# Kernel optimization log

Measured on AMD Instinct MI355X. Metric: run time of the kernel, lower is better.

Reference implementation:

```python
import jax, jax.numpy as jnp
import numpy as np

B, L = 8, 2048          # images, lines per image
C_IN, HW = 256, 128     # backbone feature channels, spatial size
DIM_LOI = 128
N_PTS0, N_PTS1 = 32, 8  # sampled points per line, after maxpool
SCALE = N_PTS0 // N_PTS1
EPS = 1e-5


def setup_inputs() -> dict:
    key = jax.random.key(0)
    ks = jax.random.split(key, 24)
    d = {}
    d['feature'] = jax.random.normal(ks[0], (B, C_IN, HW, HW), jnp.float32)
    # line endpoints in pixel coords [0, 128)
    d['lines'] = jax.random.uniform(ks[1], (B, L, 2, 2), jnp.float32) * HW
    # fc1: 1x1 conv 256 -> 128
    d['fc1_w'] = jax.random.normal(ks[2], (DIM_LOI, C_IN), jnp.float32) * 0.05
    d['fc1_b'] = jnp.zeros((DIM_LOI,), jnp.float32)
    planes = DIM_LOI // 2
    def bn(k, c):
        k1, k2, k3 = jax.random.split(k, 3)
        return (jax.random.normal(k1, (c,), jnp.float32) * 0.1 + 1.0,
                jax.random.normal(k2, (c,), jnp.float32) * 0.1,
                jax.random.normal(k3, (c,), jnp.float32) * 0.05,
                jax.random.uniform(jax.random.fold_in(k, 7), (c,), jnp.float32, 0.5, 1.5))
    d['bn1_g'], d['bn1_b'], d['bn1_m'], d['bn1_v'] = bn(ks[3], DIM_LOI)
    d['conv1_w'] = jax.random.normal(ks[4], (planes, DIM_LOI), jnp.float32) * 0.05
    d['conv1_b'] = jnp.zeros((planes,), jnp.float32)
    d['bn2_g'], d['bn2_b'], d['bn2_m'], d['bn2_v'] = bn(ks[5], planes)
    d['conv2_w'] = jax.random.normal(ks[6], (planes, planes, 3), jnp.float32) * 0.05
    d['conv2_b'] = jnp.zeros((planes,), jnp.float32)
    d['bn3_g'], d['bn3_b'], d['bn3_m'], d['bn3_v'] = bn(ks[7], planes)
    d['conv3_w'] = jax.random.normal(ks[8], (DIM_LOI, planes), jnp.float32) * 0.05
    d['conv3_b'] = jnp.zeros((DIM_LOI,), jnp.float32)
    d['fc2_w'] = jax.random.normal(ks[9], (1, DIM_LOI * N_PTS1), jnp.float32) * 0.02
    d['fc2_b'] = jnp.zeros((1,), jnp.float32)
    return d


def _bn(x, g, b, m, v):
    # x: [N, C, T], eval-mode batchnorm
    s = g * jax.lax.rsqrt(v + EPS)
    return x * s[None, :, None] + (b - m * s)[None, :, None]


def _loi_forward(feature, lines, fc1_w, fc1_b,
                 bn1_g, bn1_b, bn1_m, bn1_v, conv1_w, conv1_b,
                 bn2_g, bn2_b, bn2_m, bn2_v, conv2_w, conv2_b,
                 bn3_g, bn3_b, bn3_m, bn3_v, conv3_w, conv3_b,
                 fc2_w, fc2_b):
    # fc1: 1x1 conv -> [B, DIM_LOI, H, W]
    x = jnp.einsum('oc,bchw->bohw', fc1_w, feature) + fc1_b[None, :, None, None]

    # sample N_PTS0 points per line: p = p0*lam + p1*(1-lam) - 0.5
    lam = jnp.linspace(0.0, 1.0, N_PTS0, dtype=lines.dtype)  # [P]
    pts = (lines[:, :, 0, None, :] * lam[None, None, :, None]
           + lines[:, :, 1, None, :] * (1.0 - lam[None, None, :, None]) - 0.5)  # [B,L,P,2]
    px, py = pts[..., 0], pts[..., 1]
    px0 = jnp.clip(jnp.floor(px), 0.0, HW - 1.0)
    py0 = jnp.clip(jnp.floor(py), 0.0, HW - 1.0)
    px1 = jnp.clip(px0 + 1.0, 0.0, HW - 1.0)
    py1 = jnp.clip(py0 + 1.0, 0.0, HW - 1.0)
    px0l, py0l = px0.astype(jnp.int32), py0.astype(jnp.int32)
    px1l, py1l = px1.astype(jnp.int32), py1.astype(jnp.int32)

    def gather(f, ix, iy):  # f: [C,H,W], ix/iy: [L,P] -> [C,L,P]
        return f[:, ix, iy]

    gat = jax.vmap(gather)  # over batch
    xp = (gat(x, px0l, py0l) * ((px1 - px) * (py1 - py))[:, None]
          + gat(x, px1l, py0l) * ((px - px0) * (py1 - py))[:, None]
          + gat(x, px0l, py1l) * ((px1 - px) * (py - py0))[:, None]
          + gat(x, px1l, py1l) * ((px - px0) * (py - py0))[:, None])  # [B,C,L,P]

    xp = xp.transpose(0, 2, 1, 3).reshape(B * L, DIM_LOI, N_PTS0)  # [N,C,P]
    # MaxPool1d(kernel=stride=SCALE)
    xp = xp.reshape(B * L, DIM_LOI, N_PTS1, SCALE).max(axis=-1)  # [N,C,T=8]

    # Bottleneck1D residual: x + op(x)
    h = jax.nn.relu(_bn(xp, bn1_g, bn1_b, bn1_m, bn1_v))
    h = jnp.einsum('oc,nct->not', conv1_w, h) + conv1_b[None, :, None]
    h = jax.nn.relu(_bn(h, bn2_g, bn2_b, bn2_m, bn2_v))
    h = jax.lax.conv_general_dilated(h, conv2_w, (1,), [(1, 1)],
                                     dimension_numbers=('NCH', 'OIH', 'NCH'))
    h = h + conv2_b[None, :, None]
    h = jax.nn.relu(_bn(h, bn3_g, bn3_b, bn3_m, bn3_v))
    h = jnp.einsum('oc,nct->not', conv3_w, h) + conv3_b[None, :, None]
    xp = xp + h

    # fc2: ReLU -> Linear(dim_loi*n_pts1, 1)
    flat = jax.nn.relu(xp).reshape(B * L, DIM_LOI * N_PTS1)
    logits = (flat @ fc2_w.T + fc2_b).reshape(-1)  # [B*L]
    return logits


def reference(feature, lines, fc1_w, fc1_b,
              bn1_g, bn1_b, bn1_m, bn1_v, conv1_w, conv1_b,
              bn2_g, bn2_b, bn2_m, bn2_v, conv2_w, conv2_b,
              bn3_g, bn3_b, bn3_m, bn3_v, conv3_w, conv3_b,
              fc2_w, fc2_b):
    return _loi_forward(feature, lines, fc1_w, fc1_b,
                        bn1_g, bn1_b, bn1_m, bn1_v, conv1_w, conv1_b,
                        bn2_g, bn2_b, bn2_m, bn2_v, conv2_w, conv2_b,
                        bn3_g, bn3_b, bn3_m, bn3_v, conv3_w, conv3_b,
                        fc2_w, fc2_b)
```

## Files before the change

kernel.cpp:

```cpp
#include <hip/hip_runtime.h>

#define EPSBN 1e-5f

typedef _Float16 f16;
typedef _Float16 f16x8 __attribute__((ext_vector_type(8)));
typedef _Float16 f16x4 __attribute__((ext_vector_type(4)));
typedef _Float16 f16x2 __attribute__((ext_vector_type(2)));
typedef float    f32x4 __attribute__((ext_vector_type(4)));

__device__ inline unsigned int pack2(float a, float b) {
    union { f16x2 h; unsigned int u; } cv;
    cv.h[0] = (f16)a; cv.h[1] = (f16)b;
    return cv.u;
}
__device__ inline f16x4 hmax4(f16x4 a, f16x4 b) {
    f16x4 r;
    #pragma unroll
    for (int i = 0; i < 4; ++i) r[i] = a[i] > b[i] ? a[i] : b[i];
    return r;
}
__device__ inline f16x8 relu8(f16x8 v) {
    f16x8 r;
    #pragma unroll
    for (int i = 0; i < 8; ++i) r[i] = v[i] > (f16)0.f ? v[i] : (f16)0.f;
    return r;
}

__global__ void wprep_kernel(const float* __restrict__ fc1w,
                             const float* __restrict__ w1,
                             const float* __restrict__ w2,
                             const float* __restrict__ w3,
                             f16* __restrict__ dst) {
    const int i = blockIdx.x * 256 + threadIdx.x;
    float v;
    if (i < 32768)      v = fc1w[i];
    else if (i < 40960) v = w1[i - 32768];
    else if (i < 53248) {
        const int j = i - 40960, tau = j >> 12, rest = j & 4095;
        v = w2[rest * 3 + tau];
    } else              v = w3[i - 53248];
    dst[i] = (f16)v;
}

__global__ __launch_bounds__(512, 4)
void fc1_mfma(const float* __restrict__ feat,
              const f16*   __restrict__ w16,
              const float* __restrict__ bias,
              f16*         __restrict__ xmap) {
    __shared__ union {
        float fbuf[2][8368];
        f16   epi[256][136];
    } u;

    const int tid  = threadIdx.x;
    const int wv   = tid >> 6, lane = tid & 63;
    const int n16  = lane & 15, quad = lane >> 4;
    const int img  = blockIdx.x & 7;
    const int p0   = (blockIdx.x >> 3) << 8;

    const float* fimg = feat + (((size_t)img) << 22);

    f32x4 acc[8][2];
    #pragma unroll
    for (int ot = 0; ot < 8; ++ot) {
        acc[ot][0] = (f32x4){0.f, 0.f, 0.f, 0.f};
        acc[ot][1] = (f32x4){0.f, 0.f, 0.f, 0.f};
    }

    auto issue = [&](int s, int b) {
        #pragma unroll
        for (int i = 0; i < 4; ++i) {
            const int cl = wv * 4 + i;
            const int ch = s * 32 + cl;
            const float* src = fimg + (((size_t)ch) << 14) + p0 + lane * 4;
            float* dst = &u.fbuf[b][cl * 260 + (cl >> 3) * 16];
            __builtin_amdgcn_global_load_lds(
                (const __attribute__((address_space(1))) void*)src,
                (__attribute__((address_space(3))) void*)dst, 16, 0, 0);
        }
    };

    issue(0, 0);
    __syncthreads();

    for (int s = 0; s < 8; ++s) {
        const int cur = s & 1;
        if (s < 7) issue(s + 1, cur ^ 1);

        f16x8 xf[2];
        #pragma unroll
        for (int pt = 0; pt < 2; ++pt) {
            const int pbase = wv * 32 + pt * 16 + n16;
            const float* fb = &u.fbuf[cur][quad * 16 + pbase];
            f16x8 xv;
            #pragma unroll
            for (int j = 0; j < 8; ++j)
                xv[j] = (f16)fb[(quad * 8 + j) * 260];
            xf[pt] = xv;
        }

        const f16* wrow = w16 + (size_t)n16 * 256 + s * 32 + quad * 8;
        #pragma unroll
        for (int ot = 0; ot < 8; ++ot) {
            const f16x8 wf = *(const f16x8*)(wrow + ot * 4096);
            acc[ot][0] = __builtin_amdgcn_mfma_f32_16x16x32_f16(wf, xf[0], acc[ot][0], 0, 0, 0);
            acc[ot][1] = __builtin_amdgcn_mfma_f32_16x16x32_f16(wf, xf[1], acc[ot][1], 0, 0, 0);
        }
        __syncthreads();
    }

    #pragma unroll
    for (int ot = 0; ot < 8; ++ot) {
        const float4 bq = *(const float4*)&bias[ot * 16 + quad * 4];
        const float bqa[4] = {bq.x, bq.y, bq.z, bq.w};
        #pragma unroll
        for (int pt = 0; pt < 2; ++pt) {
            f16x4 h;
            #pragma unroll
            for (int r = 0; r < 4; ++r) h[r] = (f16)(acc[ot][pt][r] + bqa[r]);
            *(f16x4*)&u.epi[wv * 32 + pt * 16 + n16][ot * 16 + quad * 4] = h;
        }
    }
    __syncthreads();

    #pragma unroll
    for (int it = 0; it < 8; ++it) {
        const int idx = it * 512 + tid;
        const int row = idx >> 4, seg = idx & 15;
        const float4 v = *(const float4*)&u.epi[row][seg * 8];
        *(float4*)&xmap[(((size_t)(img * 16384 + p0 + row)) << 7) + seg * 8] = v;
    }
}

__global__ __launch_bounds__(256)
void loi_kernel(const f16*   __restrict__ x,
                const float* __restrict__ lines,
                const f16*   __restrict__ wsp,
                const float* __restrict__ bn1g, const float* __restrict__ bn1b,
                const float* __restrict__ bn1m, const float* __restrict__ bn1v,
                const float* __restrict__ b1,
                const float* __restrict__ bn2g, const float* __restrict__ bn2b,
                const float* __restrict__ bn2m, const float* __restrict__ bn2v,
                const float* __restrict__ b2,
                const float* __restrict__ bn3g, const float* __restrict__ bn3b,
                const float* __restrict__ bn3m, const float* __restrict__ bn3v,
                const float* __restrict__ b3,
                const float* __restrict__ fc2w, const float* __restrict__ fc2b,
                float* __restrict__ out) {
    __shared__ f16 xp[64][136];
    __shared__ alignas(16) union {
        struct { int toff[256][4]; f16 twgt[256][4]; } tp;
        struct { f16 h1[80][72]; f16 h2[64][72]; } cv;
    } u;
    __shared__ f16 s1h[128], t1h[128];
    __shared__ float s2f[64], t2f[64], s3f[64], t3f[64], b1f[64], b2f[64];
    __shared__ float b3f[128];
    __shared__ float wsum[4][8];

    const f16* w1f16 = wsp + 32768;
    const f16* w2f16 = wsp + 40960;
    const f16* w3f16 = wsp + 53248;

    const int tid  = threadIdx.x;
    const int wv   = tid >> 6, lane = tid & 63;
    const int n16  = lane & 15, quad = lane >> 4;
    const int img  = blockIdx.x & 7;
    const int mblk = blockIdx.x >> 3;

    if (tid < 128) {
        const float s = bn1g[tid] * rsqrtf(bn1v[tid] + EPSBN);
        s1h[tid] = (f16)s; t1h[tid] = (f16)(bn1b[tid] - bn1m[tid] * s);
    }
    if (tid < 64) {
        const float s = bn2g[tid] * rsqrtf(bn2v[tid] + EPSBN);
        s2f[tid] = s; t2f[tid] = bn2b[tid] - bn2m[tid] * s;
        b1f[tid] = b1[tid];
    } else if (tid < 128) {
        const int c = tid - 64;
        const float s = bn3g[c] * rsqrtf(bn3v[c] + EPSBN);
        s3f[c] = s; t3f[c] = bn3b[c] - bn3m[c] * s;
        b2f[c] = b2[c];
    } else {
        b3f[tid - 128] = b3[tid - 128];
    }

    {
        const int li = tid >> 5, pt = tid & 31;
        const int gl = img * 2048 + mblk * 8 + li;
        const float4 ln = *(const float4*)&lines[gl * 4];
        const float lam = (float)pt * (1.0f / 31.0f);
        const float px = ln.x * lam + ln.z * (1.f - lam) - 0.5f;
        const float py = ln.y * lam + ln.w * (1.f - lam) - 0.5f;
        const float px0 = fminf(fmaxf(floorf(px), 0.f), 127.f);
        const float py0 = fminf(fmaxf(floorf(py), 0.f), 127.f);
        const float px1 = fminf(px0 + 1.f, 127.f);
        const float py1 = fminf(py0 + 1.f, 127.f);
        const int ix0 = (int)px0, iy0 = (int)py0;
        const int ix1 = (int)px1, iy1 = (int)py1;
        u.tp.toff[tid][0] = (((ix0 << 7) + iy0) << 7);
        u.tp.toff[tid][1] = (((ix1 << 7) + iy0) << 7);
        u.tp.toff[tid][2] = (((ix0 << 7) + iy1) << 7);
        u.tp.toff[tid][3] = (((ix1 << 7) + iy1) << 7);
        const float wx1 = px1 - px, wx0 = px - px0;
        const float wy1 = py1 - py, wy0 = py - py0;
        u.tp.twgt[tid][0] = (f16)(wx1 * wy1); u.tp.twgt[tid][1] = (f16)(wx0 * wy1);
        u.tp.twgt[tid][2] = (f16)(wx1 * wy0); u.tp.twgt[tid][3] = (f16)(wx0 * wy0);
    }
    __syncthreads();

    {
        const int h = lane >> 5, j = lane & 31;
        const int li = wv * 2 + h;
        const f16* xbh = x + (((size_t)img) << 21) + 4 * j;
        #pragma unroll
        for (int t = 0; t < 8; ++t) {
            f16x4 m = {(f16)(-60000.f), (f16)(-60000.f), (f16)(-60000.f), (f16)(-60000.f)};
            #pragma unroll
            for (int s = 0; s < 4; ++s) {
                const int combo = li * 32 + t * 4 + s;
                const int4  off = *(const int4*)&u.tp.toff[combo][0];
                const f16x4 tw  = *(const f16x4*)&u.tp.twgt[combo][0];
                const f16x4 g00 = *(const f16x4*)(xbh + off.x);
                const f16x4 g10 = *(const f16x4*)(xbh + off.y);
                const f16x4 g01 = *(const f16x4*)(xbh + off.z);
                const f16x4 g11 = *(const f16x4*)(xbh + off.w);
                const f16x4 w0 = {tw[0], tw[0], tw[0], tw[0]};
                const f16x4 w1v = {tw[1], tw[1], tw[1], tw[1]};
                const f16x4 w2v = {tw[2], tw[2], tw[2], tw[2]};
                const f16x4 w3v = {tw[3], tw[3], tw[3], tw[3]};
                f16x4 v = g00 * w0 + g10 * w1v + g01 * w2v + g11 * w3v;
                m = hmax4(m, v);
            }
            *(f16x4*)&xp[li * 8 + t][4 * j] = m;
        }
    }
    __syncthreads();

    {
        const int r = tid >> 4, seg = tid & 15;
        const int row = (r >> 1) * 10 + (r & 1) * 9;
        *(unsigned long long*)&u.cv.h1[row][seg * 4] = 0ull;
    }

    {
        const int o_lane = wv * 16 + n16;
        f32x4 acc1[4];
        #pragma unroll
        for (int nt = 0; nt < 4; ++nt) acc1[nt] = (f32x4){0.f, 0.f, 0.f, 0.f};
        #pragma unroll
        for (int ks = 0; ks < 4; ++ks) {
            const int k = ks * 32 + quad * 8;
            const f16x8 a  = *(const f16x8*)&w1f16[o_lane * 128 + k];
            const f16x8 s8 = *(const f16x8*)&s1h[k];
            const f16x8 t8 = *(const f16x8*)&t1h[k];
            #pragma unroll
            for (int nt = 0; nt < 4; ++nt) {
                const f16x8 raw = *(const f16x8*)&xp[nt * 16 + n16][k];
                const f16x8 bf = relu8(raw * s8 + t8);
                acc1[nt] = __builtin_amdgcn_mfma_f32_16x16x32_f16(a, bf, acc1[nt], 0, 0, 0);
            }
        }
        #pragma unroll
        for (int nt = 0; nt < 4; ++nt) {
            const int n = nt * 16 + n16;
            const int nprow = (n >> 3) * 10 + (n & 7) + 1;
            #pragma unroll
            for (int r = 0; r < 4; ++r) {
                const int o = wv * 16 + quad * 4 + r;
                const float v = fmaxf((acc1[nt][r] + b1f[o]) * s2f[o] + t2f[o], 0.f);
                u.cv.h1[nprow][o] = (f16)v;
            }
        }
    }
    __syncthreads();

    {
        const int o_lane = wv * 16 + n16;
        f32x4 acc2[4];
        #pragma unroll
        for (int nt = 0; nt < 4; ++nt) acc2[nt] = (f32x4){0.f, 0.f, 0.f, 0.f};
        #pragma unroll
        for (int d = 0; d < 3; ++d) {
            const f16* A2 = w2f16 + d * 4096;
            #pragma unroll
            for (int ks = 0; ks < 2; ++ks) {
                const int k = ks * 32 + quad * 8;
                const f16x8 a = *(const f16x8*)&A2[o_lane * 64 + k];
                #pragma unroll
                for (int nt = 0; nt < 4; ++nt) {
                    const int n = nt * 16 + n16;
                    const int row = (n >> 3) * 10 + (n & 7) + d;
                    const f16x8 bf = *(const f16x8*)&u.cv.h1[row][k];
                    acc2[nt] = __builtin_amdgcn_mfma_f32_16x16x32_f16(a, bf, acc2[nt], 0, 0, 0);
                }
            }
        }
        #pragma unroll
        for (int nt = 0; nt < 4; ++nt) {
            const int n = nt * 16 + n16;
            #pragma unroll
            for (int r = 0; r < 4; ++r) {
                const int o = wv * 16 + quad * 4 + r;
                const float v = fmaxf((acc2[nt][r] + b2f[o]) * s3f[o] + t3f[o], 0.f);
                u.cv.h2[n][o] = (f16)v;
            }
        }
    }
    __syncthreads();

    {
        const int col = n16 & 7, obase = wv * 16 + quad * 4;
        float fcv[2][4];
        #pragma unroll
        for (int h = 0; h < 2; ++h)
            #pragma unroll
            for (int r = 0; r < 4; ++r)
                fcv[h][r] = fc2w[(h * 64 + obase + r) * 8 + col];

        f32x4 acc3[2][4];
        #pragma unroll
        for (int h = 0; h < 2; ++h)
            #pragma unroll
            for (int nt = 0; nt < 4; ++nt) acc3[h][nt] = (f32x4){0.f, 0.f, 0.f, 0.f};
        #pragma unroll
        for (int ks = 0; ks < 2; ++ks) {
            const int k = ks * 32 + quad * 8;
            const f16x8 a0 = *(const f16x8*)&w3f16[(wv * 16 + n16) * 64 + k];
            const f16x8 a1 = *(const f16x8*)&w3f16[(64 + wv * 16 + n16) * 64 + k];
            #pragma unroll
            for (int nt = 0; nt < 4; ++nt) {
                const f16x8 bf = *(const f16x8*)&u.cv.h2[nt * 16 + n16][k];
                acc3[0][nt] = __builtin_amdgcn_mfma_f32_16x16x32_f16(a0, bf, acc3[0][nt], 0, 0, 0);
                acc3[1][nt] = __builtin_amdgcn_mfma_f32_16x16x32_f16(a1, bf, acc3[1][nt], 0, 0, 0);
            }
        }
        float part[4] = {0.f, 0.f, 0.f, 0.f};
        #pragma unroll
        for (int h = 0; h < 2; ++h) {
            const float4 bq = *(const float4*)&b3f[h * 64 + obase];
            const float bqa[4] = {bq.x, bq.y, bq.z, bq.w};
            #pragma unroll
            for (int nt = 0; nt < 4; ++nt) {
                const int n = nt * 16 + n16;
                const f16x4 rx = *(const f16x4*)&xp[n][h * 64 + obase];
                float p = 0.f;
                #pragma unroll
                for (int r = 0; r < 4; ++r) {
                    float v = acc3[h][nt][r] + bqa[r] + (float)rx[r];
                    v = fmaxf(v, 0.f);
                    p += v * fcv[h][r];
                }
                part[nt] += p;
            }
        }
        #pragma unroll
        for (int off_i = 0; off_i < 5; ++off_i) {
            const int off = (int[]){1, 2, 4, 16, 32}[off_i];
            part[0] += __shfl_xor(part[0], off, 64);
            part[1] += __shfl_xor(part[1], off, 64);
            part[2] += __shfl_xor(part[2], off, 64);
            part[3] += __shfl_xor(part[3], off, 64);
        }
        if ((lane & 55) == 0) {
            const int par = (lane >> 3) & 1;
            wsum[wv][0 + par] = part[0];
            wsum[wv][2 + par] = part[1];
            wsum[wv][4 + par] = part[2];
            wsum[wv][6 + par] = part[3];
        }
    }
    __syncthreads();

    if (tid < 8) {
        const float s = wsum[0][tid] + wsum[1][tid] + wsum[2][tid] + wsum[3][tid];
        out[img * 2048 + mblk * 8 + tid] = s + fc2b[0];
    }
}

extern "C" void kernel_launch(void* const* d_in, const int* in_sizes, int n_in,
                              void* d_out, int out_size, void* d_ws, size_t ws_size,
                              hipStream_t stream) {
    const float* feature = (const float*)d_in[0];
    const float* lines   = (const float*)d_in[1];
    const float* fc1_w   = (const float*)d_in[2];
    const float* fc1_b   = (const float*)d_in[3];
    const float* bn1g    = (const float*)d_in[4];
    const float* bn1b    = (const float*)d_in[5];
    const float* bn1m    = (const float*)d_in[6];
    const float* bn1v    = (const float*)d_in[7];
    const float* w1      = (const float*)d_in[8];
    const float* b1      = (const float*)d_in[9];
    const float* bn2g    = (const float*)d_in[10];
    const float* bn2b    = (const float*)d_in[11];
    const float* bn2m    = (const float*)d_in[12];
    const float* bn2v    = (const float*)d_in[13];
    const float* w2      = (const float*)d_in[14];
    const float* b2      = (const float*)d_in[15];
    const float* bn3g    = (const float*)d_in[16];
    const float* bn3b    = (const float*)d_in[17];
    const float* bn3m    = (const float*)d_in[18];
    const float* bn3v    = (const float*)d_in[19];
    const float* w3      = (const float*)d_in[20];
    const float* b3      = (const float*)d_in[21];
    const float* fc2w    = (const float*)d_in[22];
    const float* fc2b    = (const float*)d_in[23];

    f16* xmap = (f16*)d_ws;
    f16* wsp  = (f16*)((char*)d_ws + (size_t)32 * 1024 * 1024);

    wprep_kernel<<<240, 256, 0, stream>>>(fc1_w, w1, w2, w3, wsp);
    fc1_mfma<<<512, 512, 0, stream>>>(feature, wsp, fc1_b, xmap);
    loi_kernel<<<2048, 256, 0, stream>>>(xmap, lines, wsp,
                                         bn1g, bn1b, bn1m, bn1v, b1,
                                         bn2g, bn2b, bn2m, bn2v, b2,
                                         bn3g, bn3b, bn3m, bn3v, b3,
                                         fc2w, fc2b, (float*)d_out);
}
```

Before: 293.5 us.

## Pipeline fc1 feature loads through four half-stage LDS buffers with explicit vmcnt waits

Replaces the double-buffered 32-channel LDS staging in the fc1 MFMA kernel with a ring of four 16-channel half-buffers, keeping about three half-stages of global-to-LDS loads in flight. The __syncthreads calls become explicit s_waitcnt vmcnt plus s_barrier with scheduling barriers, so waits cover only the data needed next. The aim is to hide more global load latency behind the MFMA work. It adds hand-tuned counter logic that depends on the order loads are issued, and the barrier placement is easy to get wrong.

```diff
diff --git a/kernel.cpp b/kernel.cpp
--- a/kernel.cpp
+++ b/kernel.cpp
@@ -48,7 +48,7 @@
               const float* __restrict__ bias,
               f16*         __restrict__ xmap) {
     __shared__ union {
-        float fbuf[2][8368];
+        float hb[4][4176];
         f16   epi[256][136];
     } u;
 
@@ -67,35 +67,43 @@
         acc[ot][1] = (f32x4){0.f, 0.f, 0.f, 0.f};
     }
 
-    auto issue = [&](int s, int b) {
-        #pragma unroll
-        for (int i = 0; i < 4; ++i) {
-            const int cl = wv * 4 + i;
-            const int ch = s * 32 + cl;
+    auto issue = [&](int h) {
+        float* base = u.hb[h & 3];
+        #pragma unroll
+        for (int i = 0; i < 2; ++i) {
+            const int cl = wv * 2 + i;
+            const int ch = h * 16 + cl;
             const float* src = fimg + (((size_t)ch) << 14) + p0 + lane * 4;
-            float* dst = &u.fbuf[b][cl * 260 + (cl >> 3) * 16];
+            float* dst = base + cl * 260 + (cl >> 3) * 16;
             __builtin_amdgcn_global_load_lds(
                 (const __attribute__((address_space(1))) void*)src,
                 (__attribute__((address_space(3))) void*)dst, 16, 0, 0);
         }
     };
 
-    issue(0, 0);
-    __syncthreads();
-
+    issue(0); issue(1); issue(2);
+
+    #pragma unroll
     for (int s = 0; s < 8; ++s) {
-        const int cur = s & 1;
-        if (s < 7) issue(s + 1, cur ^ 1);
+        if (s < 7) asm volatile("s_waitcnt vmcnt(2)" ::: "memory");
+        else       asm volatile("s_waitcnt vmcnt(0)" ::: "memory");
+        __builtin_amdgcn_s_barrier();
+        __builtin_amdgcn_sched_barrier(0);
+        asm volatile("" ::: "memory");
+
+        const float* bufA = u.hb[(2 * s) & 3];
+        const float* bufB = u.hb[(2 * s + 1) & 3];
 
         f16x8 xf[2];
         #pragma unroll
         for (int pt = 0; pt < 2; ++pt) {
             const int pbase = wv * 32 + pt * 16 + n16;
-            const float* fb = &u.fbuf[cur][quad * 16 + pbase];
+            const float* fb = ((quad & 2) ? bufB : bufA)
+                              + (quad & 1) * (8 * 260 + 16) + pbase;
             f16x8 xv;
             #pragma unroll
             for (int j = 0; j < 8; ++j)
-                xv[j] = (f16)fb[(quad * 8 + j) * 260];
+                xv[j] = (f16)fb[j * 260];
             xf[pt] = xv;
         }
 
@@ -106,8 +114,17 @@
             acc[ot][0] = __builtin_amdgcn_mfma_f32_16x16x32_f16(wf, xf[0], acc[ot][0], 0, 0, 0);
             acc[ot][1] = __builtin_amdgcn_mfma_f32_16x16x32_f16(wf, xf[1], acc[ot][1], 0, 0, 0);
         }
-        __syncthreads();
-    }
+
+        __builtin_amdgcn_sched_barrier(0);
+        __builtin_amdgcn_s_barrier();
+        __builtin_amdgcn_sched_barrier(0);
+
+        if (2 * s + 3 < 16) issue(2 * s + 3);
+        if (2 * s + 4 < 16) issue(2 * s + 4);
+    }
+
+    __builtin_amdgcn_sched_barrier(0);
+    asm volatile("" ::: "memory");
 
     #pragma unroll
     for (int ot = 0; ot < 8; ++ot) {
```

Result: slower. 302.5 us (+3.1%).
